# Optimization experiments

Measured on AMD Instinct MI355X. Metric: run time of the kernel, lower is better.

The kernel has to match this reference:

```python
import jax, jax.numpy as jnp
import numpy as np

EMB_DIM = 256
NUM_EMB = 1024
COMMITMENT = 0.25
DECAY = 0.9
EPS = 1e-5
B, H, W = 32, 64, 64


def setup_inputs() -> dict:
    key = jax.random.key(0)
    k1, k2 = jax.random.split(key)
    x = jax.random.normal(k1, (B, EMB_DIM, H, W), dtype=jnp.float32)
    embed = jax.random.normal(k2, (EMB_DIM, NUM_EMB), dtype=jnp.float32)
    cluster_size = jnp.zeros((NUM_EMB,), dtype=jnp.float32)
    ema_embed = embed  # registered as embed.clone() in the torch module
    return {"x": x, "embed": embed, "cluster_size": cluster_size, "ema_embed": ema_embed}


def reference(x, embed, cluster_size, ema_embed):
    # x: [B, C, H, W] -> [B, H, W, C]
    xp = jnp.transpose(x, (0, 2, 3, 1))
    flat = xp.reshape(-1, EMB_DIM)  # [N, D]
    # squared-distance matrix [N, K]
    dist = (jnp.sum(flat * flat, axis=1, keepdims=True)
            - 2.0 * (flat @ embed)
            + jnp.sum(embed * embed, axis=0, keepdims=True))
    embed_idx_flat = jnp.argmin(dist, axis=1)  # [N]
    embed_idx = embed_idx_flat.reshape(xp.shape[:-1])  # [B, H, W]
    quantize = embed.T[embed_idx]  # gather -> [B, H, W, D]

    # training-mode EMA codebook update (buffer updates in torch)
    ref_count = jax.ops.segment_sum(jnp.ones_like(embed_idx_flat, dtype=flat.dtype),
                                    embed_idx_flat, num_segments=NUM_EMB)  # [K]
    new_cluster_size = cluster_size * DECAY + (1.0 - DECAY) * ref_count
    n = jnp.sum(new_cluster_size)
    smoothing = n * ((new_cluster_size + EPS) / (n + new_cluster_size * EPS))
    # dw = flatten^T @ onehot, computed as a segment sum: [K, D] -> [D, K]
    dw = jax.ops.segment_sum(flat, embed_idx_flat, num_segments=NUM_EMB).T
    new_ema_embed = ema_embed * DECAY + (1.0 - DECAY) * dw
    new_embed = new_ema_embed / smoothing[None, :]

    e_latent_loss = jnp.mean((jax.lax.stop_gradient(quantize) - xp) ** 2)
    loss = COMMITMENT * e_latent_loss
    # straight-through estimator
    quantize_st = xp + jax.lax.stop_gradient(quantize - xp)
    out = jnp.transpose(quantize_st, (0, 3, 1, 2))  # [B, C, H, W]
    return out, loss, embed_idx, new_embed, new_cluster_size, new_ema_embed
```

## Files before the change

kernel.cpp:

```cpp
#include <hip/hip_runtime.h>
#include <cfloat>
#include <cstdint>

typedef unsigned short u16;

#define NTOK   131072
#define DIM    256
#define NCODE  1024
#define HW     4096
#define PLANE  1048576
#define DECAYF 0.9f
#define EPSF   1e-5f

#define O_OUT     0
#define O_LOSS    33554432
#define O_IDX     33554433
#define O_NEWEMB  33685505
#define O_NCS     33947649
#define O_NEE     33948673

#define P_XS      0
#define P_V1      16777216
#define P_V2      17825792
#define P_KK      18874368
#define P_VF      19922944
#define P_BT      22151168
#define P_ENORM64 22413312
#define P_HLIST   22415360

#define WS_ENORM  0
#define WS_CNT    1024
#define WS_LOSS   2048
#define WS_RC     2049
#define WS_RC2    2050
#define WS_LIST   2051
#define WS_SMOOTH 34819

#define REF_CAP 32768
#define DELTA   0.25f
#define MARGIN  0.03f
#define RT      16
#define DWC     64

typedef __attribute__((ext_vector_type(8))) short bf16x8;
typedef __attribute__((ext_vector_type(4))) float f32x4;

__device__ __forceinline__ u16 bf16_rne(float f) {
    unsigned int u = __float_as_uint(f);
    unsigned int r = u + 0x7FFF + ((u >> 16) & 1);
    return (u16)(r >> 16);
}
__device__ __forceinline__ float bf16_to_f(u16 s) {
    return __uint_as_float(((unsigned int)s) << 16);
}
__device__ __forceinline__ void gload_lds16(const void* g, void* l) {
    __builtin_amdgcn_global_load_lds(
        (const __attribute__((address_space(1))) unsigned int*)g,
        (__attribute__((address_space(3))) unsigned int*)l, 16, 0, 0);
}

__global__ void k_enorm(const float* __restrict__ embed, float* __restrict__ enorm,
                        double* __restrict__ enorm64) {
    int k = blockIdx.x * 256 + threadIdx.x;
    double s = 0.0;
    for (int d = 0; d < DIM; ++d) {
        float e = embed[(size_t)d * NCODE + k];
        s += (double)e * (double)e;
    }
    enorm[k] = (float)s;
    enorm64[k] = s;
}

__global__ __launch_bounds__(256) void k_xs(const float* __restrict__ x,
                                            u16* __restrict__ Xs,
                                            float* __restrict__ loss_acc)
{
    __shared__ float tile[64 * 65];
    __shared__ float red[256];
    const int tid = threadIdx.x;
    const int blk = blockIdx.x;
    const int b = blk >> 8;
    const int dc = (blk >> 6) & 3;
    const int hwc = blk & 63;
    const int d0 = dc * 64, hw0 = hwc * 64;
    const int r = tid >> 2, s = tid & 3;
    float sq = 0.f;
#pragma unroll
    for (int j = 0; j < 4; ++j) {
        float4 v = *(const float4*)&x[(size_t)b * PLANE + (size_t)(d0 + r) * HW + hw0 + s * 16 + j * 4];
        int c = s * 16 + j * 4;
        tile[r * 65 + c + 0] = v.x; tile[r * 65 + c + 1] = v.y;
        tile[r * 65 + c + 2] = v.z; tile[r * 65 + c + 3] = v.w;
        sq = fmaf(v.x, v.x, sq); sq = fmaf(v.y, v.y, sq);
        sq = fmaf(v.z, v.z, sq); sq = fmaf(v.w, v.w, sq);
    }
    __syncthreads();
    const int tk = tid >> 2, dq = tid & 3;
    u16 us[16];
#pragma unroll
    for (int j = 0; j < 16; ++j)
        us[j] = bf16_rne(tile[(dq * 16 + j) * 65 + tk]);
    size_t ob = (size_t)(b * 4096 + hw0 + tk) * 256 + d0 + dq * 16;
    *(uint4*)&Xs[ob]     = *(uint4*)&us[0];
    *(uint4*)&Xs[ob + 8] = *(uint4*)&us[8];
    red[tid] = sq; __syncthreads();
    for (int st = 128; st > 0; st >>= 1) {
        if (tid < st) red[tid] += red[tid + st];
        __syncthreads();
    }
    if (tid == 0) atomicAdd(loss_acc, red[0]);
}

__global__ __launch_bounds__(256) void k_bt(const float* __restrict__ embed, u16* __restrict__ Bt)
{
    const int tile = blockIdx.x;
    const int cc = tile >> 4, kc = tile & 15;
    const int seg = kc >> 3, dbase = (kc & 7) * 32;
    const int tid = threadIdx.x;
#pragma unroll
    for (int g2 = 0; g2 < 2; ++g2) {
        int p = g2 * 256 + tid;
        int n = p >> 2, s = p & 3, lg = (s - n) & 3;
        int code = cc * 128 + n;
        u16 us[8];
#pragma unroll
        for (int e = 0; e < 8; ++e) {
            int d = dbase + lg * 8 + e;
            float E = embed[(size_t)d * NCODE + code];
            u16 hi = bf16_rne(E);
            us[e] = seg ? bf16_rne(E - bf16_to_f(hi)) : hi;
        }
        *(uint4*)&Bt[(size_t)tile * 4096 + (size_t)p * 8] = *(uint4*)&us[0];
    }
}

__global__ __launch_bounds__(256) void k_dist(
    const u16* __restrict__ Xs, const u16* __restrict__ Bt,
    const float* __restrict__ enorm,
    float* __restrict__ pv1, float* __restrict__ pv2, float* __restrict__ pkk)
{
    __shared__ __align__(16) u16 lds[24576];
    const int tid = threadIdx.x;
    const int w = tid >> 6, l = tid & 63;
    const int xcd = blockIdx.x & 7;
    const int q = blockIdx.x >> 3;
    const int cc = q & 7;
    const int n0 = ((q >> 3) * 8 + xcd) * 128;
    const int mh = w & 1, nh = w >> 1;
    const int lane15 = l & 15, quad = l >> 4;

    const u16* src[6];
    int dstoff[6];
#pragma unroll
    for (int r = 0; r < 6; ++r) {
        int p = r * 256 + w * 64 + l;
        dstoff[r] = (r * 256 + w * 64) * 8;
        if (p < 512) {
            int m = p >> 2, s = p & 3, lg = (s - m) & 3;
            src[r] = Xs + (size_t)(n0 + m) * 256 + lg * 8;
        } else {
            int qq2 = p - 512;
            int kcb = (qq2 >> 9) * 8;
            int qq = qq2 & 511;
            src[r] = Bt + (size_t)(cc * 16 + kcb) * 4096 + (size_t)qq * 8;
        }
    }

#define STAGE_K(kc8_, buf_) do {                                              \
    _Pragma("unroll")                                                         \
    for (int r_ = 0; r_ < 6; ++r_) {                                          \
        const u16* s_ = src[r_] + (r_ < 2 ? (size_t)(kc8_) * 32               \
                                          : (size_t)(kc8_) * 4096);           \
        gload_lds16(s_, &lds[(buf_) * 12288 + dstoff[r_]]);                   \
    } } while (0)

    f32x4 acc[4][4];
#pragma unroll
    for (int i = 0; i < 4; ++i)
#pragma unroll
        for (int j = 0; j < 4; ++j) acc[i][j] = (f32x4)0.f;

    STAGE_K(0, 0);

#pragma unroll 1
    for (int kc8 = 0; kc8 < 8; ++kc8) {
        asm volatile("s_waitcnt vmcnt(0)" ::: "memory");
        __builtin_amdgcn_s_barrier();
        asm volatile("" ::: "memory");

        if (kc8 < 7) STAGE_K(kc8 + 1, (kc8 + 1) & 1);

        const u16* buf = &lds[(kc8 & 1) * 12288];
        bf16x8 af[4];
#pragma unroll
        for (int mt = 0; mt < 4; ++mt) {
            int m = mh * 64 + mt * 16 + lane15;
            int slot = (quad + m) & 3;
            af[mt] = *(const bf16x8*)&buf[(size_t)(m * 4 + slot) * 8];
        }
#pragma unroll
        for (int seg = 0; seg < 2; ++seg) {
#pragma unroll
            for (int nt = 0; nt < 4; ++nt) {
                int n = nh * 64 + nt * 16 + lane15;
                int slot = (quad + n) & 3;
                bf16x8 bfr = *(const bf16x8*)&buf[(size_t)(512 + seg * 512 + n * 4 + slot) * 8];
#pragma unroll
                for (int mt = 0; mt < 4; ++mt)
                    acc[mt][nt] = __builtin_amdgcn_mfma_f32_16x16x32_bf16(af[mt], bfr, acc[mt][nt], 0, 0, 0);
            }
        }
    }
#undef STAGE_K

    float ev[4]; int ec[4];
#pragma unroll
    for (int nt = 0; nt < 4; ++nt) {
        ec[nt] = cc * 128 + nh * 64 + nt * 16 + lane15;
        ev[nt] = enorm[ec[nt]];
    }
    float r1[4][4], r2[4][4]; int rk[4][4];
#pragma unroll
    for (int mt = 0; mt < 4; ++mt)
#pragma unroll
        for (int rg = 0; rg < 4; ++rg) {
            float v1 = FLT_MAX, v2 = FLT_MAX; int k1 = 1 << 30;
#pragma unroll
            for (int nt = 0; nt < 4; ++nt) {
                float d = fmaf(-2.f, acc[mt][nt][rg], ev[nt]);
                if (d < v1) { v2 = v1; v1 = d; k1 = ec[nt]; }
                else v2 = fminf(v2, d);
            }
            r1[mt][rg] = v1; r2[mt][rg] = v2; rk[mt][rg] = k1;
        }
#pragma unroll
    for (int mask = 1; mask <= 8; mask <<= 1) {
#pragma unroll
        for (int mt = 0; mt < 4; ++mt)
#pragma unroll
            for (int rg = 0; rg < 4; ++rg) {
                float ov1 = __shfl_xor(r1[mt][rg], mask);
                float ov2 = __shfl_xor(r2[mt][rg], mask);
                int   ok  = __shfl_xor(rk[mt][rg], mask);
                if (ov1 < r1[mt][rg] || (ov1 == r1[mt][rg] && ok < rk[mt][rg])) {
                    r2[mt][rg] = fminf(r1[mt][rg], ov2);
                    r1[mt][rg] = ov1; rk[mt][rg] = ok;
                } else {
                    r2[mt][rg] = fminf(r2[mt][rg], ov1);
                }
            }
    }
    __syncthreads();
    float* epi = (float*)lds;
    if (lane15 == 0) {
#pragma unroll
        for (int mt = 0; mt < 4; ++mt)
#pragma unroll
            for (int rg = 0; rg < 4; ++rg) {
                int t = mh * 64 + mt * 16 + quad * 4 + rg;
                float* p = &epi[(nh * 128 + t) * 3];
                p[0] = r1[mt][rg]; p[1] = r2[mt][rg]; p[2] = __int_as_float(rk[mt][rg]);
            }
    }
    __syncthreads();
    if (tid < 128) {
        const float* p0 = &epi[tid * 3];
        const float* p1 = &epi[(128 + tid) * 3];
        float v1 = p0[0], v2 = p0[1]; int k1 = __float_as_int(p0[2]);
        float a1 = p1[0], a2 = p1[1]; int ak = __float_as_int(p1[2]);
        if (a1 < v1 || (a1 == v1 && ak < k1)) { v2 = fminf(v1, a2); v1 = a1; k1 = ak; }
        else v2 = fminf(v2, a1);
        size_t o = (size_t)cc * NTOK + n0 + tid;
        pv1[o] = v1; pv2[o] = v2; pkk[o] = (float)k1;
    }
}

__global__ __launch_bounds__(256) void k_amin(
    const float* __restrict__ pv1, const float* __restrict__ pv2, const float* __restrict__ pkk,
    float* __restrict__ out_idx, float* __restrict__ vf, float* __restrict__ loss_acc,
    int* __restrict__ refcnt, int* __restrict__ reflist)
{
    const int n = blockIdx.x * 256 + threadIdx.x;
    float v1 = FLT_MAX, v2 = FLT_MAX; int k1 = 1 << 30;
    for (int cc = 0; cc < 8; ++cc) {
        float a1 = pv1[(size_t)cc * NTOK + n], a2 = pv2[(size_t)cc * NTOK + n];
        int ak = (int)pkk[(size_t)cc * NTOK + n];
        if (a1 < v1 || (a1 == v1 && ak < k1)) { v2 = fminf(v1, a2); v1 = a1; k1 = ak; }
        else v2 = fminf(v2, a1);
    }
    out_idx[n] = (float)k1;
    vf[n] = v1;
    if (v2 - v1 < DELTA) {
        int pos = atomicAdd(refcnt, 1);
        if (pos < REF_CAP) reflist[pos] = n;
    }
    __shared__ float red[256];
    red[threadIdx.x] = v1; __syncthreads();
    for (int s = 128; s > 0; s >>= 1) {
        if (threadIdx.x < s) red[threadIdx.x] += red[threadIdx.x + s];
        __syncthreads();
    }
    if (threadIdx.x == 0) atomicAdd(loss_acc, red[0]);
}

__global__ __launch_bounds__(256) void k_ref32(
    const float* __restrict__ x, const float* __restrict__ embed,
    const float* __restrict__ enorm,
    float* __restrict__ out_idx, const int* __restrict__ refcnt,
    const int* __restrict__ reflist, const float* __restrict__ vf,
    float* __restrict__ loss_acc, int* __restrict__ hardcnt, int* __restrict__ hardlist)
{
    __shared__ float xm2t[DIM][RT + 1];
    __shared__ int toks[RT];
    __shared__ float wv1[4][RT], wv2[4][RT];
    __shared__ int wk1[4][RT];
    const int tid = threadIdx.x;
    const int w = tid >> 6;
    const int cnt = min(*refcnt, REF_CAP);
    for (int base = blockIdx.x * RT; base < cnt; base += gridDim.x * RT) {
        const int nb = min(RT, cnt - base);
        for (int j = 0; j < nb; ++j) {
            int n = reflist[base + j];
            if (tid == 0) toks[j] = n;
            int b = n >> 12, hw = n & 4095;
            xm2t[tid][j] = -2.f * x[(size_t)b * PLANE + (size_t)tid * HW + hw];
        }
        if (nb < RT)
            for (int j = nb; j < RT; ++j) xm2t[tid][j] = 0.f;
        __syncthreads();

        float b1[RT], b2[RT]; int k1[RT];
#pragma unroll
        for (int j = 0; j < RT; ++j) { b1[j] = FLT_MAX; b2[j] = FLT_MAX; k1[j] = 1 << 30; }
#pragma unroll 1
        for (int c = 0; c < 4; ++c) {
            const int k = c * 256 + tid;
            float acc[RT];
#pragma unroll
            for (int j = 0; j < RT; ++j) acc[j] = 0.f;
#pragma unroll 1
            for (int d0 = 0; d0 < DIM; d0 += 8) {
                float er[8];
#pragma unroll
                for (int dd = 0; dd < 8; ++dd)
                    er[dd] = embed[(size_t)(d0 + dd) * NCODE + k];
#pragma unroll
                for (int dd = 0; dd < 8; ++dd)
#pragma unroll
                    for (int j = 0; j < RT; ++j)
                        acc[j] = fmaf(er[dd], xm2t[d0 + dd][j], acc[j]);
            }
            float e2 = enorm[k];
#pragma unroll
            for (int j = 0; j < RT; ++j) {
                float dist = e2 + acc[j];
                if (dist < b1[j]) { b2[j] = b1[j]; b1[j] = dist; k1[j] = k; }
                else b2[j] = fminf(b2[j], dist);
            }
        }

#pragma unroll
        for (int m = 1; m < 64; m <<= 1) {
#pragma unroll
            for (int j = 0; j < RT; ++j) {
                float ov1 = __shfl_xor(b1[j], m);
                float ov2 = __shfl_xor(b2[j], m);
                int   ok  = __shfl_xor(k1[j], m);
                if (ov1 < b1[j] || (ov1 == b1[j] && ok < k1[j])) {
                    b2[j] = fminf(b1[j], ov2); b1[j] = ov1; k1[j] = ok;
                } else {
                    b2[j] = fminf(b2[j], ov1);
                }
            }
        }
        if ((tid & 63) == 0) {
#pragma unroll
            for (int j = 0; j < RT; ++j) { wv1[w][j] = b1[j]; wk1[w][j] = k1[j]; wv2[w][j] = b2[j]; }
        }
        __syncthreads();
        if (tid < nb) {
            float v1 = wv1[0][tid], v2 = wv2[0][tid]; int kk = wk1[0][tid];
#pragma unroll
            for (int wi = 1; wi < 4; ++wi) {
                float a1 = wv1[wi][tid], a2 = wv2[wi][tid]; int ak = wk1[wi][tid];
                if (a1 < v1 || (a1 == v1 && ak < kk)) { v2 = fminf(v1, a2); v1 = a1; kk = ak; }
                else v2 = fminf(v2, a1);
            }
            int n = toks[tid];
            if (v2 - v1 > MARGIN) {
                out_idx[n] = (float)kk;
                atomicAdd(loss_acc, v1 - vf[n]);
            } else {
                int pos = atomicAdd(hardcnt, 1);
                hardlist[pos] = n;
            }
        }
        __syncthreads();
    }
}

__global__ __launch_bounds__(256) void k_ref64(
    const float* __restrict__ x, const float* __restrict__ embed,
    const double* __restrict__ enorm64,
    float* __restrict__ out_idx, const int* __restrict__ hcnt,
    const int* __restrict__ hlist, const float* __restrict__ vf,
    float* __restrict__ loss_acc)
{
    __shared__ float xs[DIM];
    __shared__ double wv[4];
    __shared__ int wk[4];
    const int tid = threadIdx.x;
    const int w = tid >> 6, l = tid & 63;
    const int cnt = min(*hcnt, REF_CAP);
    for (int it = blockIdx.x; it < cnt; it += gridDim.x) {
        const int n = hlist[it];
        const int b = n >> 12, hw = n & 4095;
        xs[tid] = x[(size_t)b * PLANE + (size_t)tid * HW + hw];
        __syncthreads();
        double bv = 1e300; int bk = 1 << 30;
#pragma unroll 1
        for (int c = 0; c < 4; ++c) {
            const int k = c * 256 + tid;
            const float* ep = embed + k;
            double acc = 0.0;
#pragma unroll 8
            for (int d = 0; d < DIM; ++d)
                acc = fma((double)ep[(size_t)d * NCODE], (double)xs[d], acc);
            double dist = enorm64[k] - 2.0 * acc;
            if (dist < bv) { bv = dist; bk = k; }
        }
#pragma unroll
        for (int m = 1; m < 64; m <<= 1) {
            double ov = __shfl_xor(bv, m);
            int ok = __shfl_xor(bk, m);
            if (ov < bv || (ov == bv && ok < bk)) { bv = ov; bk = ok; }
        }
        if (l == 0) { wv[w] = bv; wk[w] = bk; }
        __syncthreads();
        if (tid == 0) {
            double v = wv[0]; int kk = wk[0];
#pragma unroll
            for (int wi = 1; wi < 4; ++wi) {
                if (wv[wi] < v || (wv[wi] == v && wk[wi] < kk)) { v = wv[wi]; kk = wk[wi]; }
            }
            out_idx[n] = (float)kk;
            atomicAdd(loss_acc, (float)(v - (double)vf[n]));
        }
        __syncthreads();
    }
}

__global__ __launch_bounds__(256) void k_cnt(const float* __restrict__ out_idx, float* __restrict__ cnt) {
    __shared__ float h[NCODE];
    const int tid = threadIdx.x;
    for (int i = tid; i < NCODE; i += 256) h[i] = 0.f;
    __syncthreads();
    const int base = blockIdx.x * 2048;
#pragma unroll
    for (int t = 0; t < 8; ++t)
        unsafeAtomicAdd(&h[(int)out_idx[base + t * 256 + tid]], 1.0f);
    __syncthreads();
    for (int i = tid; i < NCODE; i += 256) {
        float v = h[i];
        if (v != 0.f) atomicAdd(&cnt[i], v);
    }
}

__global__ __launch_bounds__(256) void k_dw(
    const float* __restrict__ x, const float* __restrict__ out_idx, float* __restrict__ part)
{
    __shared__ float tile[NCODE * 9];
    const int tid = threadIdx.x;
    const int slice = blockIdx.x & 31;
    const int chunk = blockIdx.x >> 5;
    const int d0 = slice * 8;
    for (int i = tid; i < NCODE * 9; i += 256) tile[i] = 0.f;
    __syncthreads();
    const int nbeg = chunk * (NTOK / DWC);
    for (int t = tid; t < NTOK / DWC; t += 256) {
        const int n = nbeg + t;
        const int b = n >> 12, hw = n & 4095;
        const int k = (int)out_idx[n];
        const float* xb = x + (size_t)b * PLANE + hw;
        float* tp = tile + k * 9;
#pragma unroll
        for (int dl = 0; dl < 8; ++dl)
            unsafeAtomicAdd(&tp[dl], xb[(size_t)(d0 + dl) * HW]);
    }
    __syncthreads();
    for (int i = tid; i < 8 * NCODE; i += 256) {
        const int dl = i >> 10, k = i & (NCODE - 1);
        part[((size_t)chunk * DIM + d0 + dl) * NCODE + k] = tile[k * 9 + dl];
    }
}

__global__ __launch_bounds__(1024) void k_fin_cs(
    const float* __restrict__ cs_in, const float* __restrict__ cnt,
    float* __restrict__ out_ncs, float* __restrict__ smooth)
{
    const int k = threadIdx.x;
    float ncs = cs_in[k] * DECAYF + (1.f - DECAYF) * cnt[k];
    out_ncs[k] = ncs;
    __shared__ float red[1024];
    red[k] = ncs; __syncthreads();
    for (int s = 512; s > 0; s >>= 1) {
        if (k < s) red[k] += red[k + s];
        __syncthreads();
    }
    float n = red[0];
    smooth[k] = n * ((ncs + EPSF) / (n + ncs * EPSF));
}

__global__ __launch_bounds__(256) void k_fin_emb(
    const float* __restrict__ ema, const float* __restrict__ part,
    const float* __restrict__ smooth, float* __restrict__ out_ne, float* __restrict__ out_nee)
{
    const int i = blockIdx.x * 256 + threadIdx.x;
    const int k = i & (NCODE - 1);
    float dw = 0.f;
    for (int c = 0; c < DWC; ++c) dw += part[(size_t)c * (DIM * NCODE) + i];
    float nee = ema[i] * DECAYF + (1.f - DECAYF) * dw;
    out_nee[i] = nee;
    out_ne[i] = nee / smooth[k];
}

__global__ __launch_bounds__(256) void k_quant(
    const float* __restrict__ embed, const float* __restrict__ out_idx, float* __restrict__ out_q)
{
    const int n = (blockIdx.x >> 2) * 256 + threadIdx.x;
    const int dc = blockIdx.x & 3;
    const int b = n >> 12, hw = n & 4095;
    const int idx = (int)out_idx[n];
    const size_t base = (size_t)b * PLANE + hw;
    const int dend = dc * 64 + 64;
    for (int d = dc * 64; d < dend; ++d)
        out_q[base + (size_t)d * HW] = embed[(size_t)d * NCODE + idx];
}

__global__ void k_loss(const float* __restrict__ loss_acc, float* __restrict__ out_loss) {
    out_loss[0] = 0.25f * loss_acc[0] / 33554432.f;
}

extern "C" void kernel_launch(void* const* d_in, const int* in_sizes, int n_in,
                              void* d_out, int out_size, void* d_ws, size_t ws_size,
                              hipStream_t stream) {
    const float* x     = (const float*)d_in[0];
    const float* embed = (const float*)d_in[1];
    const float* csz   = (const float*)d_in[2];
    const float* ema   = (const float*)d_in[3];
    float* out = (float*)d_out;
    float* ws  = (float*)d_ws;

    u16* Xs = (u16*)(out + P_XS);
    u16* Bt = (u16*)(out + P_BT);
    double* enorm64 = (double*)(out + P_ENORM64);

    hipMemsetAsync(ws + WS_CNT, 0, (size_t)(WS_RC2 + 1 - WS_CNT) * sizeof(float), stream);

    k_enorm<<<4, 256, 0, stream>>>(embed, ws + WS_ENORM, enorm64);
    k_xs<<<8192, 256, 0, stream>>>(x, Xs, ws + WS_LOSS);
    k_bt<<<128, 256, 0, stream>>>(embed, Bt);
    k_dist<<<8192, 256, 0, stream>>>(Xs, Bt, ws + WS_ENORM,
                                     out + P_V1, out + P_V2, out + P_KK);
    k_amin<<<NTOK / 256, 256, 0, stream>>>(out + P_V1, out + P_V2, out + P_KK,
                                           out + O_IDX, out + P_VF, ws + WS_LOSS,
                                           (int*)(ws + WS_RC), (int*)(ws + WS_LIST));
    k_ref32<<<2048, 256, 0, stream>>>(x, embed, ws + WS_ENORM, out + O_IDX,
                                      (const int*)(ws + WS_RC), (const int*)(ws + WS_LIST),
                                      out + P_VF, ws + WS_LOSS,
                                      (int*)(ws + WS_RC2), (int*)(out + P_HLIST));
    k_ref64<<<2048, 256, 0, stream>>>(x, embed, enorm64, out + O_IDX,
                                      (const int*)(ws + WS_RC2), (const int*)(out + P_HLIST),
                                      out + P_VF, ws + WS_LOSS);
    k_cnt<<<64, 256, 0, stream>>>(out + O_IDX, ws + WS_CNT);
    k_dw<<<32 * DWC, 256, 0, stream>>>(x, out + O_IDX, out + P_XS);
    k_fin_cs<<<1, 1024, 0, stream>>>(csz, ws + WS_CNT, out + O_NCS, ws + WS_SMOOTH);
    k_fin_emb<<<1024, 256, 0, stream>>>(ema, out + P_XS, ws + WS_SMOOTH,
                                        out + O_NEWEMB, out + O_NEE);
    k_quant<<<NTOK / 256 * 4, 256, 0, stream>>>(embed, out + O_IDX, out + O_OUT);
    k_loss<<<1, 1, 0, stream>>>(ws + WS_LOSS, out + O_LOSS);
}
```

Baseline: 1.109 ms.

## Enlarge distance GEMM tile to 256 tokens and drop LDS double buffering

The distance kernel now covers 256 tokens per block instead of 128, with each wave holding an 8x4 MFMA accumulator tile. This doubles reuse of each codebook fragment and halves the number of blocks. LDS double buffering is replaced by a single buffer with two barriers per K step, and the LDS swizzle adds an (m>>2) term to cut bank conflicts; k_bt is changed to write the matching layout. The cost is higher register pressure (launch_bounds 256,2) and global-load latency that is no longer hidden behind compute.

```diff
diff --git a/kernel.cpp b/kernel.cpp
--- a/kernel.cpp
+++ b/kernel.cpp
@@ -120,7 +120,7 @@
 #pragma unroll
     for (int g2 = 0; g2 < 2; ++g2) {
         int p = g2 * 256 + tid;
-        int n = p >> 2, s = p & 3, lg = (s - n) & 3;
+        int n = p >> 2, s = p & 3, lg = (s - n - (n >> 2)) & 3;
         int code = cc * 128 + n;
         u16 us[8];
 #pragma unroll
@@ -134,84 +134,74 @@
     }
 }
 
-__global__ __launch_bounds__(256) void k_dist(
+__global__ __launch_bounds__(256, 2) void k_dist(
     const u16* __restrict__ Xs, const u16* __restrict__ Bt,
     const float* __restrict__ enorm,
     float* __restrict__ pv1, float* __restrict__ pv2, float* __restrict__ pkk)
 {
-    __shared__ __align__(16) u16 lds[24576];
+    __shared__ __align__(16) u16 lds[16384];
     const int tid = threadIdx.x;
     const int w = tid >> 6, l = tid & 63;
     const int xcd = blockIdx.x & 7;
     const int q = blockIdx.x >> 3;
     const int cc = q & 7;
-    const int n0 = ((q >> 3) * 8 + xcd) * 128;
+    const int n0 = ((q >> 3) * 8 + xcd) * 256;
     const int mh = w & 1, nh = w >> 1;
     const int lane15 = l & 15, quad = l >> 4;
 
-    const u16* src[6];
-    int dstoff[6];
-#pragma unroll
-    for (int r = 0; r < 6; ++r) {
-        int p = r * 256 + w * 64 + l;
-        dstoff[r] = (r * 256 + w * 64) * 8;
-        if (p < 512) {
-            int m = p >> 2, s = p & 3, lg = (s - m) & 3;
+    const u16* src[8];
+    u16* dstp[8];
+#pragma unroll
+    for (int r = 0; r < 8; ++r) {
+        int p = r * 256 + tid;
+        int pbase = r * 256 + w * 64;
+        if (r < 4) {
+            int m = p >> 2, s = p & 3, lg = (s - m - (m >> 2)) & 3;
             src[r] = Xs + (size_t)(n0 + m) * 256 + lg * 8;
+            dstp[r] = &lds[(size_t)pbase * 8];
         } else {
-            int qq2 = p - 512;
-            int kcb = (qq2 >> 9) * 8;
-            int qq = qq2 & 511;
-            src[r] = Bt + (size_t)(cc * 16 + kcb) * 4096 + (size_t)qq * 8;
-        }
-    }
-
-#define STAGE_K(kc8_, buf_) do {                                              \
-    _Pragma("unroll")                                                         \
-    for (int r_ = 0; r_ < 6; ++r_) {                                          \
-        const u16* s_ = src[r_] + (r_ < 2 ? (size_t)(kc8_) * 32               \
-                                          : (size_t)(kc8_) * 4096);           \
-        gload_lds16(s_, &lds[(buf_) * 12288 + dstoff[r_]]);                   \
-    } } while (0)
-
-    f32x4 acc[4][4];
-#pragma unroll
-    for (int i = 0; i < 4; ++i)
+            int q2 = p - 1024;
+            int segi = q2 >> 9, pos = q2 & 511;
+            src[r] = Bt + (size_t)(cc * 16 + segi * 8) * 4096 + (size_t)pos * 8;
+            dstp[r] = &lds[8192 + (size_t)(pbase - 1024) * 8];
+        }
+    }
+
+    f32x4 acc[8][4];
+#pragma unroll
+    for (int i = 0; i < 8; ++i)
 #pragma unroll
         for (int j = 0; j < 4; ++j) acc[i][j] = (f32x4)0.f;
 
-    STAGE_K(0, 0);
-
-#pragma unroll 1
     for (int kc8 = 0; kc8 < 8; ++kc8) {
-        asm volatile("s_waitcnt vmcnt(0)" ::: "memory");
-        __builtin_amdgcn_s_barrier();
-        asm volatile("" ::: "memory");
-
-        if (kc8 < 7) STAGE_K(kc8 + 1, (kc8 + 1) & 1);
-
-        const u16* buf = &lds[(kc8 & 1) * 12288];
-        bf16x8 af[4];
-#pragma unroll
-        for (int mt = 0; mt < 4; ++mt) {
-            int m = mh * 64 + mt * 16 + lane15;
-            int slot = (quad + m) & 3;
-            af[mt] = *(const bf16x8*)&buf[(size_t)(m * 4 + slot) * 8];
+        __syncthreads();
+#pragma unroll
+        for (int r = 0; r < 8; ++r) {
+            const u16* s = src[r] + (r < 4 ? (size_t)kc8 * 32 : (size_t)kc8 * 4096);
+            gload_lds16(s, dstp[r]);
+        }
+        __syncthreads();
+
+        bf16x8 af[8];
+#pragma unroll
+        for (int mt = 0; mt < 8; ++mt) {
+            int m = mh * 128 + mt * 16 + lane15;
+            int slot = (quad + m + (m >> 2)) & 3;
+            af[mt] = *(const bf16x8*)&lds[(size_t)(m * 4 + slot) * 8];
         }
 #pragma unroll
         for (int seg = 0; seg < 2; ++seg) {
 #pragma unroll
             for (int nt = 0; nt < 4; ++nt) {
                 int n = nh * 64 + nt * 16 + lane15;
-                int slot = (quad + n) & 3;
-                bf16x8 bfr = *(const bf16x8*)&buf[(size_t)(512 + seg * 512 + n * 4 + slot) * 8];
-#pragma unroll
-                for (int mt = 0; mt < 4; ++mt)
+                int slot = (quad + n + (n >> 2)) & 3;
+                bf16x8 bfr = *(const bf16x8*)&lds[8192 + seg * 4096 + (size_t)(n * 4 + slot) * 8];
+#pragma unroll
+                for (int mt = 0; mt < 8; ++mt)
                     acc[mt][nt] = __builtin_amdgcn_mfma_f32_16x16x32_bf16(af[mt], bfr, acc[mt][nt], 0, 0, 0);
             }
         }
     }
-#undef STAGE_K
 
     float ev[4]; int ec[4];
 #pragma unroll
@@ -219,9 +209,11 @@
         ec[nt] = cc * 128 + nh * 64 + nt * 16 + lane15;
         ev[nt] = enorm[ec[nt]];
     }
-    float r1[4][4], r2[4][4]; int rk[4][4];
-#pragma unroll
-    for (int mt = 0; mt < 4; ++mt)
+    __syncthreads();
+    float* epi = (float*)lds;
+#pragma unroll
+    for (int mt = 0; mt < 8; ++mt) {
+        float r1[4], r2[4]; int rk[4];
 #pragma unroll
         for (int rg = 0; rg < 4; ++rg) {
             float v1 = FLT_MAX, v2 = FLT_MAX; int k1 = 1 << 30;
@@ -231,41 +223,36 @@
                 if (d < v1) { v2 = v1; v1 = d; k1 = ec[nt]; }
                 else v2 = fminf(v2, d);
             }
-            r1[mt][rg] = v1; r2[mt][rg] = v2; rk[mt][rg] = k1;
-        }
-#pragma unroll
-    for (int mask = 1; mask <= 8; mask <<= 1) {
-#pragma unroll
-        for (int mt = 0; mt < 4; ++mt)
+            r1[rg] = v1; r2[rg] = v2; rk[rg] = k1;
+        }
+#pragma unroll
+        for (int mask = 1; mask <= 8; mask <<= 1) {
 #pragma unroll
             for (int rg = 0; rg < 4; ++rg) {
-                float ov1 = __shfl_xor(r1[mt][rg], mask);
-                float ov2 = __shfl_xor(r2[mt][rg], mask);
-                int   ok  = __shfl_xor(rk[mt][rg], mask);
-                if (ov1 < r1[mt][rg] || (ov1 == r1[mt][rg] && ok < rk[mt][rg])) {
-                    r2[mt][rg] = fminf(r1[mt][rg], ov2);
-                    r1[mt][rg] = ov1; rk[mt][rg] = ok;
+                float ov1 = __shfl_xor(r1[rg], mask);
+                float ov2 = __shfl_xor(r2[rg], mask);
+                int   ok  = __shfl_xor(rk[rg], mask);
+                if (ov1 < r1[rg] || (ov1 == r1[rg] && ok < rk[rg])) {
+                    r2[rg] = fminf(r1[rg], ov2);
+                    r1[rg] = ov1; rk[rg] = ok;
                 } else {
-                    r2[mt][rg] = fminf(r2[mt][rg], ov1);
+                    r2[rg] = fminf(r2[rg], ov1);
                 }
             }
-    }
-    __syncthreads();
-    float* epi = (float*)lds;
-    if (lane15 == 0) {
-#pragma unroll
-        for (int mt = 0; mt < 4; ++mt)
+        }
+        if (lane15 == 0) {
 #pragma unroll
             for (int rg = 0; rg < 4; ++rg) {
-                int t = mh * 64 + mt * 16 + quad * 4 + rg;
-                float* p = &epi[(nh * 128 + t) * 3];
-                p[0] = r1[mt][rg]; p[1] = r2[mt][rg]; p[2] = __int_as_float(rk[mt][rg]);
-            }
-    }
-    __syncthreads();
-    if (tid < 128) {
+                int t = mh * 128 + mt * 16 + quad * 4 + rg;
+                float* pp = &epi[(nh * 256 + t) * 3];
+                pp[0] = r1[rg]; pp[1] = r2[rg]; pp[2] = __int_as_float(rk[rg]);
+            }
+        }
+    }
+    __syncthreads();
+    {
         const float* p0 = &epi[tid * 3];
-        const float* p1 = &epi[(128 + tid) * 3];
+        const float* p1 = &epi[(256 + tid) * 3];
         float v1 = p0[0], v2 = p0[1]; int k1 = __float_as_int(p0[2]);
         float a1 = p1[0], a2 = p1[1]; int ak = __float_as_int(p1[2]);
         if (a1 < v1 || (a1 == v1 && ak < k1)) { v2 = fminf(v1, a2); v1 = a1; k1 = ak; }
@@ -560,7 +547,7 @@
     k_enorm<<<4, 256, 0, stream>>>(embed, ws + WS_ENORM, enorm64);
     k_xs<<<8192, 256, 0, stream>>>(x, Xs, ws + WS_LOSS);
     k_bt<<<128, 256, 0, stream>>>(embed, Bt);
-    k_dist<<<8192, 256, 0, stream>>>(Xs, Bt, ws + WS_ENORM,
+    k_dist<<<4096, 256, 0, stream>>>(Xs, Bt, ws + WS_ENORM,
                                      out + P_V1, out + P_V2, out + P_KK);
     k_amin<<<NTOK / 256, 256, 0, stream>>>(out + P_V1, out + P_V2, out + P_KK,
                                            out + O_IDX, out + P_VF, ws + WS_LOSS,
```

Result: faster. 1.040 ms (-6.2%).
